# Optimization experiments

Hardware: AMD Instinct MI355X
Metric: run time of the kernel (lower is better)

## Reference

```python
import jax, jax.numpy as jnp
import numpy as np

B, N, F_IN, F_OUT, E = 8, 2048, 512, 256, 5
ALPHA = 0.2  # leaky relu slope
NEG = -9e15


def setup_inputs() -> dict:
    key = jax.random.key(0)
    ks = jax.random.split(key, 11)
    s_in = 1.0 / np.sqrt(F_IN)
    s_out = 1.0 / np.sqrt(F_OUT)
    s_e = 1.0 / np.sqrt(E)
    return {
        "feat": jax.random.normal(ks[0], (B, N, F_IN), jnp.float32),
        "adj": jax.random.randint(ks[1], (B, N, N), 0, 2, jnp.int32),
        "W": jax.random.normal(ks[2], (F_IN, F_OUT), jnp.float32) * s_in,
        "W_1": jax.random.normal(ks[3], (F_IN, F_OUT), jnp.float32) * s_in,
        "W_2": jax.random.normal(ks[4], (F_IN, F_OUT), jnp.float32) * s_in,
        "a_1": jax.random.normal(ks[5], (F_OUT, 1), jnp.float32) * s_out,
        "a_2": jax.random.normal(ks[6], (F_OUT, 1), jnp.float32) * s_out,
        "a_12": jax.random.normal(ks[7], (F_OUT, F_OUT), jnp.float32) * s_out,
        "L_w": jax.random.normal(ks[8], (E, F_IN), jnp.float32) * s_in,
        "R_w": jax.random.normal(ks[9], (E, F_IN), jnp.float32) * s_in,
        "B_w": jax.random.normal(ks[10], (F_OUT, E, E), jnp.float32) * s_e,
    }


def reference(feat, adj, W, W_1, W_2, a_1, a_2, a_12, L_w, R_w, B_w):
    # --- attention ---
    h = jnp.einsum('bnf,fd->bnd', feat, W)                 # [B,N,D]
    Ax = jnp.einsum('bnd,do->bno', h, a_1)[..., 0]         # [B,N] (score of target)
    Ay = jnp.einsum('bnd,do->bno', h, a_2)[..., 0]         # [B,N] (score of source)
    A_xy = jnp.einsum('bid,de,bje->bij', h, a_12, h)       # [B,N,N] bilinear term
    logits = Ax[:, None, :] + Ay[:, :, None] + A_xy        # [B,N,N]
    e = jnp.where(logits > 0, logits, ALPHA * logits)      # leaky relu
    e = jnp.where(adj > 0, e, NEG)
    attention = jax.nn.softmax(e, axis=-1)                 # dropout p=0 / eval -> identity
    # --- aggregate ---
    feat_agg = jnp.einsum('bij,bjf->bif', attention, feat) # [B,N,F_IN]
    # --- update ---
    h_1 = jnp.einsum('bnf,fd->bnd', feat, W_1)
    h_2 = jnp.einsum('bnf,fd->bnd', feat_agg, W_2)
    e1 = jnp.einsum('bnf,ef->bne', feat, L_w)              # [B,N,E]
    e2 = jnp.einsum('bnf,ef->bne', feat_agg, R_w)          # [B,N,E]
    h_12 = jnp.einsum('bni,oij,bnj->bno', e1, B_w, e2)     # [B,N,F_OUT]
    return h_1 + h_2 + h_12  # activation=None -> identity
```

## Files before the change

### kernel.cpp

```cpp
#include <hip/hip_runtime.h>
#include <hip/hip_bf16.h>

#define BB 8
#define NN 2048
#define FIN 512
#define FOUT 256
#define EE 5
#define ALPHA_ 0.2f
#define NEGV -9e15f
#define JW 512

typedef __hip_bfloat16 bf16;
typedef __bf16 bf16x8 __attribute__((ext_vector_type(8)));
typedef float f32x4 __attribute__((ext_vector_type(4)));
typedef unsigned long long u64;

__device__ __forceinline__ float bf2f(bf16 x) { return __bfloat162float(x); }
__device__ __forceinline__ bf16 f2bf(float x) { return __float2bfloat16(x); }

__device__ __forceinline__ void async16(const bf16* g, bf16* l) {
    __builtin_amdgcn_global_load_lds(
        (const __attribute__((address_space(1))) void*)g,
        (__attribute__((address_space(3))) void*)l, 16, 0, 0);
}


__global__ void split_f32_bf16(const float* __restrict__ in,
                               bf16* __restrict__ hi, bf16* __restrict__ lo) {
    long i = ((long)blockIdx.x * blockDim.x + threadIdx.x) * 8;
    float4 a = *(const float4*)(&in[i]);
    float4 b = *(const float4*)(&in[i + 4]);
    float x[8] = { a.x, a.y, a.z, a.w, b.x, b.y, b.z, b.w };
    bf16 th[8], tl[8];
    for (int k = 0; k < 8; k++) {
        th[k] = f2bf(x[k]);
        tl[k] = f2bf(x[k] - bf2f(th[k]));
    }
    *(uint4*)(&hi[i]) = *(const uint4*)th;
    *(uint4*)(&lo[i]) = *(const uint4*)tl;
}

__global__ void pack_adj(const int* __restrict__ adj, u64* __restrict__ adjm) {
    long wid = (((long)blockIdx.x * 256) + threadIdx.x) >> 6;
    int lane = threadIdx.x & 63;
    long base = wid * 256;
    for (int c = 0; c < 4; c++) {
        int a = adj[base + c * 64 + lane];
        u64 m = __ballot(a > 0);
        if (lane == 0) adjm[base / 64 + c] = m;
    }
}

__global__ void transpose_split(const float* __restrict__ in,
                                bf16* __restrict__ hi, bf16* __restrict__ lo,
                                int R, int C) {
    __shared__ bf16 th[32][33], tl[32][33];
    int c0 = blockIdx.x * 32, r0 = blockIdx.y * 32;
    int x = threadIdx.x, y = threadIdx.y;
    for (int k = 0; k < 4; k++) {
        int r = y + k * 8;
        float f = in[(long)(r0 + r) * C + c0 + x];
        bf16 h = f2bf(f);
        th[r][x] = h;
        tl[r][x] = f2bf(f - bf2f(h));
    }
    __syncthreads();
    for (int k = 0; k < 4; k++) {
        int r = y + k * 8;
        hi[(long)(c0 + r) * R + r0 + x] = th[x][r];
        lo[(long)(c0 + r) * R + r0 + x] = tl[x][r];
    }
}

__global__ void transpose_f32_bf16(const float* __restrict__ in, bf16* __restrict__ out,
                                   int R, int C, long sin_b, long sout_b) {
    __shared__ bf16 tile[32][33];
    long bi = (long)blockIdx.z * sin_b;
    long bo = (long)blockIdx.z * sout_b;
    int c0 = blockIdx.x * 32, r0 = blockIdx.y * 32;
    int x = threadIdx.x, y = threadIdx.y;
    for (int k = 0; k < 4; k++) {
        int r = y + k * 8;
        tile[r][x] = f2bf(in[bi + (long)(r0 + r) * C + c0 + x]);
    }
    __syncthreads();
    for (int k = 0; k < 4; k++) {
        int r = y + k * 8;
        out[bo + (long)(c0 + r) * R + r0 + x] = tile[x][r];
    }
}

__global__ __launch_bounds__(256) void gemm_bt_split(
        const bf16* __restrict__ Ah, const bf16* __restrict__ Al,
        const bf16* __restrict__ Bh, const bf16* __restrict__ Bl,
        bf16* __restrict__ Chi, bf16* __restrict__ Clo,
        const float* __restrict__ bias, int Nn, int K) {
    __shared__ alignas(16) bf16 Ash[2][128 * 32], Asl[2][128 * 32];
    __shared__ alignas(16) bf16 Bsh[2][128 * 32], Bsl[2][128 * 32];
    int tid = threadIdx.x;
    int lane = tid & 63, ww = tid >> 6;
    int wm = ww >> 1, wn = ww & 1;
    int quad = lane >> 4, l16 = lane & 15;
    int qx = quad ^ ((l16 >> 1) & 3);
    int sseg = (tid & 3) ^ ((tid >> 3) & 3);
    int m0 = blockIdx.x * 128, n0 = blockIdx.y * 128;
    f32x4 acc[4][4] = {};
    auto STAGE = [&](int k0, int buf) {
#pragma unroll
        for (int i = 0; i < 2; i++) {
            int idx = tid + i * 256;
            int row = idx >> 2;
            long ao = (long)(m0 + row) * K + k0 + sseg * 8;
            long bo = (long)(n0 + row) * K + k0 + sseg * 8;
            async16(&Ah[ao], &Ash[buf][idx * 8]);
            async16(&Al[ao], &Asl[buf][idx * 8]);
            async16(&Bh[bo], &Bsh[buf][idx * 8]);
            async16(&Bl[bo], &Bsl[buf][idx * 8]);
        }
    };
    int nk = K / 32;
    STAGE(0, 0);
    for (int s = 0; s < nk; s += 2) {
#pragma unroll
        for (int u = 0; u < 2; u++) {
            int step = s + u;
            if (step + 1 < nk) STAGE((step + 1) * 32, u ^ 1);
            if (step + 1 < nk) asm volatile("s_waitcnt vmcnt(8)" ::: "memory");
            else               asm volatile("s_waitcnt vmcnt(0)" ::: "memory");
            __builtin_amdgcn_s_barrier();
            __builtin_amdgcn_sched_barrier(0);
            __builtin_amdgcn_s_setprio(1);
            bf16x8 afh[4], afl[4], bfh[4], bfl[4];
#pragma unroll
            for (int mi = 0; mi < 4; mi++) {
                int so = (wm * 64 + mi * 16 + l16) * 32 + qx * 8;
                afh[mi] = *(const bf16x8*)(&Ash[u][so]);
                afl[mi] = *(const bf16x8*)(&Asl[u][so]);
            }
#pragma unroll
            for (int ni = 0; ni < 4; ni++) {
                int so = (wn * 64 + ni * 16 + l16) * 32 + qx * 8;
                bfh[ni] = *(const bf16x8*)(&Bsh[u][so]);
                bfl[ni] = *(const bf16x8*)(&Bsl[u][so]);
            }
#pragma unroll
            for (int mi = 0; mi < 4; mi++)
#pragma unroll
                for (int ni = 0; ni < 4; ni++) {
                    acc[mi][ni] = __builtin_amdgcn_mfma_f32_16x16x32_bf16(afh[mi], bfh[ni], acc[mi][ni], 0, 0, 0);
                    acc[mi][ni] = __builtin_amdgcn_mfma_f32_16x16x32_bf16(afh[mi], bfl[ni], acc[mi][ni], 0, 0, 0);
                    acc[mi][ni] = __builtin_amdgcn_mfma_f32_16x16x32_bf16(afl[mi], bfh[ni], acc[mi][ni], 0, 0, 0);
                }
            __builtin_amdgcn_s_setprio(0);
            __builtin_amdgcn_sched_barrier(0);
            __builtin_amdgcn_s_barrier();
            __builtin_amdgcn_sched_barrier(0);
        }
    }
    for (int mi = 0; mi < 4; mi++)
        for (int ni = 0; ni < 4; ni++) {
            int col = n0 + wn * 64 + ni * 16 + l16;
            float bv = bias ? bias[col] : 0.f;
            for (int r = 0; r < 4; r++) {
                int row = m0 + wm * 64 + mi * 16 + quad * 4 + r;
                float v = acc[mi][ni][r] + bv;
                bf16 h = f2bf(v);
                Chi[(long)row * Nn + col] = h;
                Clo[(long)row * Nn + col] = f2bf(v - bf2f(h));
            }
        }
}

__global__ __launch_bounds__(256) void gemm_bt(
        const bf16* __restrict__ A, const bf16* __restrict__ Bt,
        bf16* __restrict__ C, int Nn, int K, long sA, long sB, long sC) {
    __shared__ alignas(16) bf16 As[2][128 * 32];
    __shared__ alignas(16) bf16 Bs[2][128 * 32];
    const bf16* Ab = A + (long)blockIdx.z * sA;
    const bf16* Bb = Bt + (long)blockIdx.z * sB;
    bf16* Cb = C + (long)blockIdx.z * sC;
    int tid = threadIdx.x;
    int lane = tid & 63, ww = tid >> 6;
    int wm = ww >> 1, wn = ww & 1;
    int quad = lane >> 4, l16 = lane & 15;
    int qx = quad ^ ((l16 >> 1) & 3);
    int sseg = (tid & 3) ^ ((tid >> 3) & 3);
    int m0 = blockIdx.x * 128, n0 = blockIdx.y * 128;
    f32x4 acc[4][4] = {};
    auto STAGE = [&](int k0, int buf) {
#pragma unroll
        for (int i = 0; i < 2; i++) {
            int idx = tid + i * 256;
            int row = idx >> 2;
            async16(&Ab[(long)(m0 + row) * K + k0 + sseg * 8], &As[buf][idx * 8]);
            async16(&Bb[(long)(n0 + row) * K + k0 + sseg * 8], &Bs[buf][idx * 8]);
        }
    };
    int nk = K / 32;
    STAGE(0, 0);
    for (int s = 0; s < nk; s += 2) {
#pragma unroll
        for (int u = 0; u < 2; u++) {
            int step = s + u;
            if (step + 1 < nk) STAGE((step + 1) * 32, u ^ 1);
            if (step + 1 < nk) asm volatile("s_waitcnt vmcnt(4)" ::: "memory");
            else               asm volatile("s_waitcnt vmcnt(0)" ::: "memory");
            __builtin_amdgcn_s_barrier();
            __builtin_amdgcn_sched_barrier(0);
            __builtin_amdgcn_s_setprio(1);
            bf16x8 af[4], bfr[4];
#pragma unroll
            for (int mi = 0; mi < 4; mi++)
                af[mi] = *(const bf16x8*)(&As[u][(wm * 64 + mi * 16 + l16) * 32 + qx * 8]);
#pragma unroll
            for (int ni = 0; ni < 4; ni++)
                bfr[ni] = *(const bf16x8*)(&Bs[u][(wn * 64 + ni * 16 + l16) * 32 + qx * 8]);
#pragma unroll
            for (int mi = 0; mi < 4; mi++)
#pragma unroll
                for (int ni = 0; ni < 4; ni++)
                    acc[mi][ni] = __builtin_amdgcn_mfma_f32_16x16x32_bf16(
                        af[mi], bfr[ni], acc[mi][ni], 0, 0, 0);
            __builtin_amdgcn_s_setprio(0);
            __builtin_amdgcn_sched_barrier(0);
            __builtin_amdgcn_s_barrier();
            __builtin_amdgcn_sched_barrier(0);
        }
    }
    for (int mi = 0; mi < 4; mi++)
        for (int ni = 0; ni < 4; ni++) {
            int col = n0 + wn * 64 + ni * 16 + l16;
            for (int r = 0; r < 4; r++) {
                int row = m0 + wm * 64 + mi * 16 + quad * 4 + r;
                Cb[(long)row * Nn + col] = f2bf(acc[mi][ni][r]);
            }
        }
}

__global__ __launch_bounds__(256) void gemm_pv(
        const bf16* __restrict__ A, const bf16* __restrict__ Bt,
        bf16* __restrict__ C, const float* __restrict__ rs,
        const float* __restrict__ fin) {
    __shared__ alignas(16) bf16 As[2][128 * 32];
    __shared__ alignas(16) bf16 Bs[2][128 * 32];
    int flat = blockIdx.x;
    int xcd = flat & 7, j = flat >> 3;
    int panel = xcd * 16 + (j >> 2);
    int b = panel >> 4;
    int m0 = (panel & 15) * 128;
    int n0 = (j & 3) * 128;
    const bf16* Ab = A + (long)b * NN * NN;
    const bf16* Bb = Bt + (long)b * FIN * NN;
    bf16* Cb = C + (long)b * NN * FIN;
    int tid = threadIdx.x;
    int lane = tid & 63, ww = tid >> 6;
    int wm = ww >> 1, wn = ww & 1;
    int quad = lane >> 4, l16 = lane & 15;
    int qx = quad ^ ((l16 >> 1) & 3);
    int sseg = (tid & 3) ^ ((tid >> 3) & 3);
    f32x4 acc[4][4] = {};
    auto STAGE = [&](int k0, int buf) {
#pragma unroll
        for (int i = 0; i < 2; i++) {
            int idx = tid + i * 256;
            int row = idx >> 2;
            async16(&Ab[(long)(m0 + row) * NN + k0 + sseg * 8], &As[buf][idx * 8]);
            async16(&Bb[(long)(n0 + row) * NN + k0 + sseg * 8], &Bs[buf][idx * 8]);
        }
    };
    const int nk = NN / 32;
    STAGE(0, 0);
    for (int s = 0; s < nk; s += 2) {
#pragma unroll
        for (int u = 0; u < 2; u++) {
            int step = s + u;
            int k0 = step * 32;
            if (k0 && !(k0 & 127)) {
                int c = k0 >> 7;
#pragma unroll
                for (int mi = 0; mi < 4; mi++) {
                    float4 rv = *(const float4*)(&rs[((long)b * 16 + c) * NN
                                                     + m0 + wm * 64 + mi * 16 + quad * 4]);
#pragma unroll
                    for (int ni = 0; ni < 4; ni++) {
                        acc[mi][ni][0] *= rv.x;
                        acc[mi][ni][1] *= rv.y;
                        acc[mi][ni][2] *= rv.z;
                        acc[mi][ni][3] *= rv.w;
                    }
                }
            }
            if (step + 1 < nk) STAGE((step + 1) * 32, u ^ 1);
            if (step + 1 < nk) asm volatile("s_waitcnt vmcnt(4)" ::: "memory");
            else               asm volatile("s_waitcnt vmcnt(0)" ::: "memory");
            __builtin_amdgcn_s_barrier();
            __builtin_amdgcn_sched_barrier(0);
            __builtin_amdgcn_s_setprio(1);
            bf16x8 af[4], bfr[4];
#pragma unroll
            for (int mi = 0; mi < 4; mi++)
                af[mi] = *(const bf16x8*)(&As[u][(wm * 64 + mi * 16 + l16) * 32 + qx * 8]);
#pragma unroll
            for (int ni = 0; ni < 4; ni++)
                bfr[ni] = *(const bf16x8*)(&Bs[u][(wn * 64 + ni * 16 + l16) * 32 + qx * 8]);
#pragma unroll
            for (int mi = 0; mi < 4; mi++)
#pragma unroll
                for (int ni = 0; ni < 4; ni++)
                    acc[mi][ni] = __builtin_amdgcn_mfma_f32_16x16x32_bf16(
                        af[mi], bfr[ni], acc[mi][ni], 0, 0, 0);
            __builtin_amdgcn_s_setprio(0);
            __builtin_amdgcn_sched_barrier(0);
            __builtin_amdgcn_s_barrier();
            __builtin_amdgcn_sched_barrier(0);
        }
    }
    for (int mi = 0; mi < 4; mi++) {
        float4 fv = *(const float4*)(&fin[(long)b * NN + m0 + wm * 64 + mi * 16 + quad * 4]);
        for (int ni = 0; ni < 4; ni++) {
            int col = n0 + wn * 64 + ni * 16 + l16;
            float fvr[4] = { fv.x, fv.y, fv.z, fv.w };
            for (int r = 0; r < 4; r++) {
                int row = m0 + wm * 64 + mi * 16 + quad * 4 + r;
                Cb[(long)row * FIN + col] = f2bf(acc[mi][ni][r] * fvr[r]);
            }
        }
    }
}

__global__ void ay_kernel(const bf16* __restrict__ hh, const bf16* __restrict__ hl,
                          const float* __restrict__ a2, float* __restrict__ Ay) {
    int lane = threadIdx.x & 63, w = threadIdx.x >> 6;
    long row = (long)blockIdx.x * 4 + w;
    float p = 0.f;
    for (int i = 0; i < 4; i++) {
        int d = i * 64 + lane;
        p += (bf2f(hh[row * FOUT + d]) + bf2f(hl[row * FOUT + d])) * a2[d];
    }
    for (int off = 32; off; off >>= 1) p += __shfl_xor(p, off);
    if (lane == 0) Ay[row] = p;
}

__global__ __launch_bounds__(256) void pass_score(
        const bf16* __restrict__ qh_, const bf16* __restrict__ ql_,
        const bf16* __restrict__ hh_, const bf16* __restrict__ hl_,
        const u64* __restrict__ adjm, const float* __restrict__ Ay,
        float* __restrict__ mpm, float* __restrict__ mpl,
        bf16* __restrict__ P) {
    __shared__ alignas(16) bf16 Hsh[2][128 * 32], Hsl[2][128 * 32];
    __shared__ alignas(16) bf16 pst[4][16 * 64];
    int tid = threadIdx.x;
    int lane = tid & 63, w = tid >> 6;
    int quad = lane >> 4, l16 = lane & 15;
    int qx = quad ^ ((l16 >> 1) & 3);
    int sseg = (tid & 3) ^ ((tid >> 3) & 3);
    int b = blockIdx.z, jz = blockIdx.y;
    int i0 = blockIdx.x * 64 + w * 16;
    long qoff = ((long)b * NN + i0) * FOUT;
    const bf16* hbh = hh_ + ((long)b * NN + (long)jz * JW) * FOUT;
    const bf16* hbl = hl_ + ((long)b * NN + (long)jz * JW) * FOUT;
    const u64* amb = adjm + ((long)b * NN + i0) * (NN / 64) + jz * (JW / 64);
    bf16* pw = pst[w];

    bf16x8 qfh[8], qfl[8];
#pragma unroll
    for (int kk = 0; kk < 8; kk++) {
        qfh[kk] = *(const bf16x8*)(&qh_[qoff + (long)l16 * FOUT + kk * 32 + quad * 8]);
        qfl[kk] = *(const bf16x8*)(&ql_[qoff + (long)l16 * FOUT + kk * 32 + quad * 8]);
    }
    float ay_[4];
#pragma unroll
    for (int r = 0; r < 4; r++) ay_[r] = Ay[(long)b * NN + i0 + quad * 4 + r];

    float m_[4], l_[4];
#pragma unroll
    for (int r = 0; r < 4; r++) { m_[r] = -3.0e38f; l_[r] = 0.f; }

    auto STAGE = [&](int jc, int kk, int buf) {
#pragma unroll
        for (int i = 0; i < 2; i++) {
            int idx = tid + i * 256;
            int row = idx >> 2;
            long go = (long)(jc * 128 + row) * FOUT + kk * 32 + sseg * 8;
            async16(&hbh[go], &Hsh[buf][idx * 8]);
            async16(&hbl[go], &Hsl[buf][idx * 8]);
        }
    };

    f32x4 sacc[8];
#pragma unroll
    for (int ni = 0; ni < 8; ni++) sacc[ni] = (f32x4){0.f, 0.f, 0.f, 0.f};

    STAGE(0, 0, 0);
    for (int jc = 0; jc < 4; jc++) {
#pragma unroll
        for (int kk = 0; kk < 8; kk++) {
            const int cur = kk & 1;
            if (kk < 7)           STAGE(jc, kk + 1, cur ^ 1);
            else if (jc < 3)      STAGE(jc + 1, 0, cur ^ 1);
            if (kk == 0) {
                if (jc == 0) asm volatile("s_waitcnt vmcnt(4)" ::: "memory");
                else         asm volatile("s_waitcnt vmcnt(8)" ::: "memory");
            } else if (kk == 7 && jc == 3) {
                asm volatile("s_waitcnt vmcnt(0)" ::: "memory");
            } else {
                asm volatile("s_waitcnt vmcnt(4)" ::: "memory");
            }
            __builtin_amdgcn_s_barrier();
            __builtin_amdgcn_sched_barrier(0);

            __builtin_amdgcn_s_setprio(1);
#pragma unroll
            for (int ni = 0; ni < 8; ni++) {
                int so = (ni * 16 + l16) * 32 + qx * 8;
                bf16x8 hfh = *(const bf16x8*)(&Hsh[cur][so]);
                bf16x8 hfl = *(const bf16x8*)(&Hsl[cur][so]);
                sacc[ni] = __builtin_amdgcn_mfma_f32_16x16x32_bf16(qfh[kk], hfh, sacc[ni], 0, 0, 0);
                sacc[ni] = __builtin_amdgcn_mfma_f32_16x16x32_bf16(qfh[kk], hfl, sacc[ni], 0, 0, 0);
                sacc[ni] = __builtin_amdgcn_mfma_f32_16x16x32_bf16(qfl[kk], hfh, sacc[ni], 0, 0, 0);
            }
            __builtin_amdgcn_s_setprio(0);

            if (kk == 7) {
                u64 am[4][2];
#pragma unroll
                for (int r = 0; r < 4; r++) {
                    am[r][0] = amb[(long)(quad * 4 + r) * (NN / 64) + jc * 2 + 0];
                    am[r][1] = amb[(long)(quad * 4 + r) * (NN / 64) + jc * 2 + 1];
                }
#pragma unroll
                for (int ni = 0; ni < 8; ni++)
#pragma unroll
                    for (int r = 0; r < 4; r++) {
                        float v = sacc[ni][r] + ay_[r];
                        v = v > 0.f ? v : ALPHA_ * v;
                        int bit = (int)((am[r][ni >> 2] >> ((ni * 16 + l16) & 63)) & 1);
                        sacc[ni][r] = bit ? v : NEGV;
                    }
#pragma unroll
                for (int r = 0; r < 4; r++) {
                    float mc = -3.0e38f;
#pragma unroll
                    for (int ni = 0; ni < 8; ni++) mc = fmaxf(mc, sacc[ni][r]);
                    for (int off = 8; off; off >>= 1) mc = fmaxf(mc, __shfl_xor(mc, off));
                    float mnew = fmaxf(m_[r], mc);
                    float scale = __expf(m_[r] - mnew);
                    float ps = 0.f;
#pragma unroll
                    for (int ni = 0; ni < 8; ni++) {
                        float p = __expf(sacc[ni][r] - mnew);
                        sacc[ni][r] = p;
                        ps += p;
                    }
                    for (int off = 8; off; off >>= 1) ps += __shfl_xor(ps, off);
                    l_[r] = l_[r] * scale + ps;
                    m_[r] = mnew;
                    if (l16 == 0)
                        mpm[(((long)b * 4 + jz) * 4 + jc) * NN + i0 + quad * 4 + r] = mnew;
                }
#pragma unroll
                for (int h = 0; h < 2; h++) {
#pragma unroll
                    for (int ni = 0; ni < 4; ni++)
#pragma unroll
                        for (int r = 0; r < 4; r++) {
                            int row = quad * 4 + r;
                            int byt = (row * 128 + (ni * 16 + l16) * 2) ^ ((row & 7) << 4);
                            *(bf16*)((char*)pw + byt) = f2bf(sacc[h * 4 + ni][r]);
                        }
#pragma unroll
                    for (int s2 = 0; s2 < 2; s2++) {
                        int cq = quad + s2 * 4;
                        int byt = (l16 * 128 + cq * 16) ^ ((l16 & 7) << 4);
                        uint4 v = *(const uint4*)((const char*)pw + byt);
                        *(uint4*)(&P[((long)b * NN + i0 + l16) * NN + (long)jz * JW
                                     + jc * 128 + h * 64 + cq * 8]) = v;
                    }
                }
#pragma unroll
                for (int ni = 0; ni < 8; ni++) sacc[ni] = (f32x4){0.f, 0.f, 0.f, 0.f};
            }
            __builtin_amdgcn_sched_barrier(0);
            __builtin_amdgcn_s_barrier();
            __builtin_amdgcn_sched_barrier(0);
        }
    }
    if (l16 == 0)
#pragma unroll
        for (int r = 0; r < 4; r++)
            mpl[((long)b * 4 + jz) * NN + i0 + quad * 4 + r] = l_[r];
}

__global__ void ml_merge(const float* __restrict__ mpm, const float* __restrict__ mpl,
                         float* __restrict__ rs, float* __restrict__ fin) {
    long row = (long)blockIdx.x * blockDim.x + threadIdx.x;
    long b = row / NN, n = row % NN;
    float mc[16];
#pragma unroll
    for (int c = 0; c < 16; c++) mc[c] = mpm[(b * 16 + c) * NN + n];
    float m = fmaxf(fmaxf(mc[3], mc[7]), fmaxf(mc[11], mc[15]));
    float l = 0.f;
#pragma unroll
    for (int jz = 0; jz < 4; jz++)
        l += mpl[(b * 4 + jz) * NN + n] * __expf(mc[jz * 4 + 3] - m);
    fin[row] = __expf(mc[15] - m) / l;
#pragma unroll
    for (int c = 1; c < 16; c++)
        rs[(b * 16 + c) * NN + n] = __expf(mc[c - 1] - mc[c]);
}

__global__ void e_kernel(const bf16* __restrict__ X, const float* __restrict__ Wt,
                         float* __restrict__ out) {
    int lane = threadIdx.x & 63, w = threadIdx.x >> 6;
    long row = (long)blockIdx.x * 4 + w;
    uint4 raw = *(const uint4*)(&X[row * FIN + lane * 8]);
    const bf16* xp = (const bf16*)&raw;
    float xv[8];
    for (int i = 0; i < 8; i++) xv[i] = bf2f(xp[i]);
    for (int e = 0; e < EE; e++) {
        float4 w0 = *(const float4*)(&Wt[e * FIN + lane * 8]);
        float4 w1 = *(const float4*)(&Wt[e * FIN + lane * 8 + 4]);
        float p = xv[0] * w0.x + xv[1] * w0.y + xv[2] * w0.z + xv[3] * w0.w
                + xv[4] * w1.x + xv[5] * w1.y + xv[6] * w1.z + xv[7] * w1.w;
        for (int off = 32; off; off >>= 1) p += __shfl_xor(p, off);
        if (lane == 0) out[row * EE + e] = p;
    }
}

__global__ void final_kernel(float* __restrict__ out,
                             const bf16* __restrict__ h1, const bf16* __restrict__ h2,
                             const float* __restrict__ e1, const float* __restrict__ e2,
                             const float* __restrict__ Bw) {
    long row = blockIdx.x;
    int o = threadIdx.x;
    float a[EE], c[EE];
    for (int i = 0; i < EE; i++) { a[i] = e1[row * EE + i]; c[i] = e2[row * EE + i]; }
    const float* bw = Bw + (long)o * EE * EE;
    float acc = 0.f;
    for (int i = 0; i < EE; i++)
        for (int j = 0; j < EE; j++)
            acc += bw[i * EE + j] * a[i] * c[j];
    long idx = row * FOUT + o;
    out[idx] = acc + bf2f(h1[idx]) + bf2f(h2[idx]);
}

extern "C" void kernel_launch(void* const* d_in, const int* in_sizes, int n_in,
                              void* d_out, int out_size, void* d_ws, size_t ws_size,
                              hipStream_t stream) {
    const float* feat = (const float*)d_in[0];
    const int*   adj  = (const int*)d_in[1];
    const float* W    = (const float*)d_in[2];
    const float* W1   = (const float*)d_in[3];
    const float* W2   = (const float*)d_in[4];
    const float* a1   = (const float*)d_in[5];
    const float* a2   = (const float*)d_in[6];
    const float* a12  = (const float*)d_in[7];
    const float* Lw   = (const float*)d_in[8];
    const float* Rw   = (const float*)d_in[9];
    const float* Bw   = (const float*)d_in[10];
    float* out = (float*)d_out;

    char* ws = (char*)d_ws;
    size_t off = 0;
    auto alloc = [&](size_t bytes) {
        char* p = ws + off;
        off += (bytes + 255) & ~(size_t)255;
        return p;
    };
    bf16* WTh  = (bf16*)alloc((size_t)FOUT * FIN * 2);
    bf16* WTl  = (bf16*)alloc((size_t)FOUT * FIN * 2);
    bf16* W1T  = (bf16*)alloc((size_t)FOUT * FIN * 2);
    bf16* W2T  = (bf16*)alloc((size_t)FOUT * FIN * 2);
    bf16* aTh  = (bf16*)alloc((size_t)FOUT * FOUT * 2);
    bf16* aTl  = (bf16*)alloc((size_t)FOUT * FOUT * 2);
    bf16* fh   = (bf16*)alloc((size_t)BB * NN * FIN * 2);
    bf16* fl   = (bf16*)alloc((size_t)BB * NN * FIN * 2);
    bf16* hh   = (bf16*)alloc((size_t)BB * NN * FOUT * 2);
    bf16* hl   = (bf16*)alloc((size_t)BB * NN * FOUT * 2);
    bf16* featT= (bf16*)alloc((size_t)BB * NN * FIN * 2);
    float* Ay  = (float*)alloc((size_t)BB * NN * 4);
    float* mpm = (float*)alloc((size_t)BB * 4 * 4 * NN * 4);
    float* mpl = (float*)alloc((size_t)BB * 4 * NN * 4);
    float* rs  = (float*)alloc((size_t)BB * 16 * NN * 4);
    float* fin = (float*)alloc((size_t)BB * NN * 4);
    float* e1  = (float*)alloc((size_t)BB * NN * EE * 4);
    float* e2  = (float*)alloc((size_t)BB * NN * EE * 4);
    u64* adjm  = (u64*)alloc((size_t)BB * NN * (NN / 64) * 8);
    bf16* P    = (bf16*)alloc((size_t)BB * NN * NN * 2);
    bf16* qh   = (bf16*)d_out;
    bf16* ql   = qh + (size_t)BB * NN * FOUT;
    bf16* fagg = fl;
    bf16* h1   = hh;
    bf16* h2   = hl;

    dim3 tb(32, 8, 1);
    split_f32_bf16<<<(BB * NN * FIN) / (256 * 8), 256, 0, stream>>>(feat, fh, fl);
    pack_adj<<<(BB * NN * NN) / (256 * 4), 256, 0, stream>>>(adj, adjm);
    transpose_split<<<dim3(FOUT / 32, FIN / 32, 1), tb, 0, stream>>>(W, WTh, WTl, FIN, FOUT);
    transpose_split<<<dim3(FOUT / 32, FOUT / 32, 1), tb, 0, stream>>>(a12, aTh, aTl, FOUT, FOUT);
    transpose_f32_bf16<<<dim3(FOUT / 32, FIN / 32, 1), tb, 0, stream>>>(W1, W1T, FIN, FOUT, 0, 0);
    transpose_f32_bf16<<<dim3(FOUT / 32, FIN / 32, 1), tb, 0, stream>>>(W2, W2T, FIN, FOUT, 0, 0);
    transpose_f32_bf16<<<dim3(FIN / 32, NN / 32, BB), tb, 0, stream>>>(
        feat, featT, NN, FIN, (long)NN * FIN, (long)FIN * NN);
    gemm_bt_split<<<dim3(BB * NN / 128, FOUT / 128, 1), 256, 0, stream>>>(
        fh, fl, WTh, WTl, hh, hl, nullptr, FOUT, FIN);
    ay_kernel<<<BB * NN / 4, 256, 0, stream>>>(hh, hl, a2, Ay);
    gemm_bt_split<<<dim3(BB * NN / 128, FOUT / 128, 1), 256, 0, stream>>>(
        hh, hl, aTh, aTl, qh, ql, a1, FOUT, FOUT);
    pass_score<<<dim3(NN / 64, 4, BB), 256, 0, stream>>>(
        qh, ql, hh, hl, adjm, Ay, mpm, mpl, P);
    ml_merge<<<(BB * NN) / 256, 256, 0, stream>>>(mpm, mpl, rs, fin);
    gemm_pv<<<dim3(512, 1, 1), 256, 0, stream>>>(
        P, featT, fagg, rs, fin);
    gemm_bt<<<dim3(BB * NN / 128, FOUT / 128, 1), 256, 0, stream>>>(
        fh, W1T, h1, FOUT, FIN, 0, 0, 0);
    gemm_bt<<<dim3(BB * NN / 128, FOUT / 128, 1), 256, 0, stream>>>(
        fagg, W2T, h2, FOUT, FIN, 0, 0, 0);
    e_kernel<<<BB * NN / 4, 256, 0, stream>>>(fh, Lw, e1);
    e_kernel<<<BB * NN / 4, 256, 0, stream>>>(fagg, Rw, e2);
    final_kernel<<<BB * NN, FOUT, 0, stream>>>(out, h1, h2, e1, e2, Bw);
}
```

Before: 519.6 us.

## Fuse feat split with transpose and remap pass_score blocks for XCD L2 locality

Merges the bf16 hi/lo split of feat and the transposed featT copy into one tiled kernel, so feat is read from global memory once instead of twice. It also flattens the pass_score grid to 1D and remaps block IDs so that blocks sharing the same (batch, j-window) H tile go to the same XCD (flat & 7). The aim is better per-XCD L2 reuse of the hh/hl window. The fused kernel does scalar, non-vectorised stores of hi/lo, which may be less efficient than the old 16-byte stores.

```diff
diff --git a/kernel.cpp b/kernel.cpp
--- a/kernel.cpp
+++ b/kernel.cpp
@@ -25,19 +25,28 @@
 }
 
 
-__global__ void split_f32_bf16(const float* __restrict__ in,
-                               bf16* __restrict__ hi, bf16* __restrict__ lo) {
-    long i = ((long)blockIdx.x * blockDim.x + threadIdx.x) * 8;
-    float4 a = *(const float4*)(&in[i]);
-    float4 b = *(const float4*)(&in[i + 4]);
-    float x[8] = { a.x, a.y, a.z, a.w, b.x, b.y, b.z, b.w };
-    bf16 th[8], tl[8];
-    for (int k = 0; k < 8; k++) {
-        th[k] = f2bf(x[k]);
-        tl[k] = f2bf(x[k] - bf2f(th[k]));
-    }
-    *(uint4*)(&hi[i]) = *(const uint4*)th;
-    *(uint4*)(&lo[i]) = *(const uint4*)tl;
+__global__ void split_transpose(const float* __restrict__ in,
+                                bf16* __restrict__ hi, bf16* __restrict__ lo,
+                                bf16* __restrict__ outT) {
+    __shared__ bf16 tile[32][33];
+    long bi = (long)blockIdx.z * NN * FIN;
+    long bo = (long)blockIdx.z * FIN * NN;
+    int c0 = blockIdx.x * 32, r0 = blockIdx.y * 32;
+    int x = threadIdx.x, y = threadIdx.y;
+    for (int k = 0; k < 4; k++) {
+        int r = y + k * 8;
+        long idx = bi + (long)(r0 + r) * FIN + c0 + x;
+        float f = in[idx];
+        bf16 h = f2bf(f);
+        hi[idx] = h;
+        lo[idx] = f2bf(f - bf2f(h));
+        tile[r][x] = h;
+    }
+    __syncthreads();
+    for (int k = 0; k < 4; k++) {
+        int r = y + k * 8;
+        outT[bo + (long)(c0 + r) * NN + r0 + x] = tile[x][r];
+    }
 }
 
 __global__ void pack_adj(const int* __restrict__ adj, u64* __restrict__ adjm) {
@@ -354,8 +363,12 @@
     int quad = lane >> 4, l16 = lane & 15;
     int qx = quad ^ ((l16 >> 1) & 3);
     int sseg = (tid & 3) ^ ((tid >> 3) & 3);
-    int b = blockIdx.z, jz = blockIdx.y;
-    int i0 = blockIdx.x * 64 + w * 16;
+    int flat = blockIdx.x;
+    int xcd = flat & 7, slot = flat >> 3;
+    int widx = slot >> 5, iblk = slot & 31;
+    int window = widx * 8 + xcd;
+    int b = window >> 2, jz = window & 3;
+    int i0 = iblk * 64 + w * 16;
     long qoff = ((long)b * NN + i0) * FOUT;
     const bf16* hbh = hh_ + ((long)b * NN + (long)jz * JW) * FOUT;
     const bf16* hbl = hl_ + ((long)b * NN + (long)jz * JW) * FOUT;
@@ -594,20 +607,18 @@
     bf16* h2   = hl;
 
     dim3 tb(32, 8, 1);
-    split_f32_bf16<<<(BB * NN * FIN) / (256 * 8), 256, 0, stream>>>(feat, fh, fl);
+    split_transpose<<<dim3(FIN / 32, NN / 32, BB), tb, 0, stream>>>(feat, fh, fl, featT);
     pack_adj<<<(BB * NN * NN) / (256 * 4), 256, 0, stream>>>(adj, adjm);
     transpose_split<<<dim3(FOUT / 32, FIN / 32, 1), tb, 0, stream>>>(W, WTh, WTl, FIN, FOUT);
     transpose_split<<<dim3(FOUT / 32, FOUT / 32, 1), tb, 0, stream>>>(a12, aTh, aTl, FOUT, FOUT);
     transpose_f32_bf16<<<dim3(FOUT / 32, FIN / 32, 1), tb, 0, stream>>>(W1, W1T, FIN, FOUT, 0, 0);
     transpose_f32_bf16<<<dim3(FOUT / 32, FIN / 32, 1), tb, 0, stream>>>(W2, W2T, FIN, FOUT, 0, 0);
-    transpose_f32_bf16<<<dim3(FIN / 32, NN / 32, BB), tb, 0, stream>>>(
-        feat, featT, NN, FIN, (long)NN * FIN, (long)FIN * NN);
     gemm_bt_split<<<dim3(BB * NN / 128, FOUT / 128, 1), 256, 0, stream>>>(
         fh, fl, WTh, WTl, hh, hl, nullptr, FOUT, FIN);
     ay_kernel<<<BB * NN / 4, 256, 0, stream>>>(hh, hl, a2, Ay);
     gemm_bt_split<<<dim3(BB * NN / 128, FOUT / 128, 1), 256, 0, stream>>>(
         hh, hl, aTh, aTl, qh, ql, a1, FOUT, FOUT);
-    pass_score<<<dim3(NN / 64, 4, BB), 256, 0, stream>>>(
+    pass_score<<<dim3(1024, 1, 1), 256, 0, stream>>>(
         qh, ql, hh, hl, adjm, Ay, mpm, mpl, P);
     ml_merge<<<(BB * NN) / 256, 256, 0, stream>>>(mpm, mpl, rs, fin);
     gemm_pv<<<dim3(512, 1, 1), 256, 0, stream>>>(
```

Result: no change. 528.8 us (+1.8%).
